# Kernel optimization log

Measured on AMD Instinct MI355X. Metric: run time of the kernel, lower is better.

The kernel has to match this reference:

```python
import jax, jax.numpy as jnp
import numpy as np

N_NODES = 50000
N_EDGES = 800000
IN_DIM = 512
HIDDEN = 512
NUM_HASH = 4
HASH_DIM = 128
NUM_GRAPHS = 64
NUM_CLASSES = 10


def _hash_mats(rng, num_hash, in_dim, hash_dim):
    # Each row of each hash matrix has a single +-1 entry at a random column.
    cols = rng.integers(0, hash_dim, size=(num_hash, in_dim))
    signs = (rng.integers(0, 2, size=(num_hash, in_dim)) * 2 - 1).astype(np.float32)
    W = np.zeros((num_hash, in_dim, hash_dim), dtype=np.float32)
    W[np.arange(num_hash)[:, None], np.arange(in_dim)[None, :], cols] = signs
    return jnp.asarray(W)


def setup_inputs() -> dict:
    key = jax.random.key(0)
    ks = jax.random.split(key, 10)
    rng = np.random.default_rng(0)
    x = jax.random.normal(ks[0], (N_NODES, IN_DIM), dtype=jnp.float32)
    edge_index = jax.random.randint(ks[1], (2, N_EDGES), 0, N_NODES, dtype=jnp.int64)
    batch = jnp.sort(jax.random.randint(ks[2], (N_NODES,), 0, NUM_GRAPHS, dtype=jnp.int64))
    s1 = 1.0 / np.sqrt(NUM_HASH * HASH_DIM)
    s2 = 1.0 / np.sqrt(IN_DIM)
    s3 = 1.0 / np.sqrt(HIDDEN)
    return {
        "x": x,
        "edge_index": edge_index,
        "batch": batch,
        "Hm1": _hash_mats(rng, NUM_HASH, IN_DIM, HASH_DIM),
        "Wp1": jax.random.normal(ks[3], (NUM_HASH * HASH_DIM, HIDDEN), dtype=jnp.float32) * s1,
        "Ws1": jax.random.normal(ks[4], (IN_DIM, HIDDEN), dtype=jnp.float32) * s2,
        "b1": jnp.zeros((HIDDEN,), dtype=jnp.float32),
        "Hm2": _hash_mats(rng, NUM_HASH, HIDDEN, HASH_DIM),
        "Wp2": jax.random.normal(ks[5], (NUM_HASH * HASH_DIM, HIDDEN), dtype=jnp.float32) * s1,
        "Ws2": jax.random.normal(ks[6], (HIDDEN, HIDDEN), dtype=jnp.float32) * s3,
        "b2": jnp.zeros((HIDDEN,), dtype=jnp.float32),
        "Wc": jax.random.normal(ks[7], (HIDDEN, NUM_CLASSES), dtype=jnp.float32) * s3,
        "bc": jnp.zeros((NUM_CLASSES,), dtype=jnp.float32),
    }


def _demo_layer(h, src, dst, deg, Hm, Wp, Ws, b):
    n = h.shape[0]
    # Degree-bucketed gather + mean == segment-mean over edges by source node.
    nsum = jax.ops.segment_sum(h[dst], src, num_segments=n)  # [N, D]
    agg = jnp.where(deg[:, None] > 0, nsum / jnp.maximum(deg, 1.0)[:, None], h)
    # Multi-hash matmul + concat: [N, K*HASH_DIM]
    hashed = jnp.einsum("nd,kdh->nkh", agg, Hm).reshape(n, -1)
    out = hashed @ Wp + h @ Ws + b
    return jax.nn.elu(out)  # dropout is identity in eval mode


def reference(x, edge_index, batch, Hm1, Wp1, Ws1, b1, Hm2, Wp2, Ws2, b2, Wc, bc):
    n = x.shape[0]
    src, dst = edge_index[0], edge_index[1]
    deg = jax.ops.segment_sum(jnp.ones(src.shape, x.dtype), src, num_segments=n)
    h = _demo_layer(x, src, dst, deg, Hm1, Wp1, Ws1, b1)
    h = _demo_layer(h, src, dst, deg, Hm2, Wp2, Ws2, b2)
    # global mean pool per graph
    cnt = jax.ops.segment_sum(jnp.ones((n,), h.dtype), batch, num_segments=NUM_GRAPHS)
    g = jax.ops.segment_sum(h, batch, num_segments=NUM_GRAPHS) / jnp.maximum(cnt, 1.0)[:, None]
    return g @ Wc + bc
```

## Files before the change

### kernel.cpp

```cpp
#include <hip/hip_runtime.h>
#include <hip/hip_bf16.h>
#include <math.h>

#define N_NODES_C 50000
#define N_EDGES_C 800000
#define DIM 512
#define NUM_GRAPHS_C 64
#define NUM_CLASSES_C 10

#define NROWT ((N_NODES_C + 127) / 128)
#define GEMM_BLOCKS (((NROWT * 4 + 31) / 32) * 32)

#define SCAN_BLK 1024
#define SCAN_NBLK ((N_NODES_C + SCAN_BLK - 1) / SCAN_BLK)

typedef short bf16x8 __attribute__((ext_vector_type(8)));
typedef float f32x4 __attribute__((ext_vector_type(4)));
typedef float f32x2 __attribute__((ext_vector_type(2)));
typedef unsigned u32x2 __attribute__((ext_vector_type(2)));

__device__ __forceinline__ float bf2f(short s) {
    return __uint_as_float(((unsigned)(unsigned short)s) << 16);
}
__device__ __forceinline__ short f2bf(float f) {
    unsigned u = __float_as_uint(f);
    u += 0x7FFF + ((u >> 16) & 1);
    return (short)(u >> 16);
}
__device__ __forceinline__ float eluf(float v) {
    return v > 0.0f ? v : expm1f(v);
}
__device__ __forceinline__ unsigned f32x4_to_fp8(float a, float b, float c, float d) {
    int w = 0;
    w = __builtin_amdgcn_cvt_pk_fp8_f32(a, b, w, false);
    w = __builtin_amdgcn_cvt_pk_fp8_f32(c, d, w, true);
    return (unsigned)w;
}
__device__ __forceinline__ unsigned char f32_to_fp8(float v) {
    return (unsigned char)(__builtin_amdgcn_cvt_pk_fp8_f32(v, v, 0, false) & 0xff);
}
__device__ __forceinline__ void acc_fp8x8(float* acc, u32x2 w) {
    f32x2 a = __builtin_amdgcn_cvt_pk_f32_fp8((int)w[0], false);
    f32x2 b = __builtin_amdgcn_cvt_pk_f32_fp8((int)w[0], true);
    f32x2 c = __builtin_amdgcn_cvt_pk_f32_fp8((int)w[1], false);
    f32x2 d = __builtin_amdgcn_cvt_pk_f32_fp8((int)w[1], true);
    acc[0] += a[0]; acc[1] += a[1]; acc[2] += b[0]; acc[3] += b[1];
    acc[4] += c[0]; acc[5] += c[1]; acc[6] += d[0]; acc[7] += d[1];
}

__device__ __forceinline__ void gl16(const void* g, void* l) {
    __builtin_amdgcn_global_load_lds(
        (const __attribute__((address_space(1))) unsigned*)g,
        (__attribute__((address_space(3))) unsigned*)l, 16, 0, 0);
}


__global__ void k_hist(const int* __restrict__ src, int* __restrict__ cnt) {
    int e = blockIdx.x * blockDim.x + threadIdx.x;
    if (e < N_EDGES_C) atomicAdd(&cnt[src[e]], 1);
}

__global__ __launch_bounds__(1024)
void k_bsum(const int* __restrict__ cnt, int* __restrict__ bsum) {
    __shared__ int sh[1024];
    int i = blockIdx.x * 1024 + threadIdx.x;
    sh[threadIdx.x] = (i < N_NODES_C) ? cnt[i] : 0;
    __syncthreads();
    for (int ofs = 512; ofs > 0; ofs >>= 1) {
        if ((int)threadIdx.x < ofs) sh[threadIdx.x] += sh[threadIdx.x + ofs];
        __syncthreads();
    }
    if (threadIdx.x == 0) bsum[blockIdx.x] = sh[0];
}

__global__ __launch_bounds__(64)
void k_bscan(const int* __restrict__ bsum, int* __restrict__ bofs,
             int* __restrict__ start) {
    int l = threadIdx.x;
    int own = (l < SCAN_NBLK) ? bsum[l] : 0;
    int v = own;
    for (int ofs = 1; ofs < 64; ofs <<= 1) {
        int t = __shfl_up(v, ofs, 64);
        if (l >= ofs) v += t;
    }
    if (l < SCAN_NBLK) bofs[l] = v - own;
    if (l == 63) start[N_NODES_C] = v;
}

__global__ __launch_bounds__(1024)
void k_scan_apply(const int* __restrict__ cnt, const int* __restrict__ bofs,
                  int* __restrict__ start, int* __restrict__ cursor) {
    __shared__ int sh[1024];
    int i = blockIdx.x * 1024 + threadIdx.x;
    int v = (i < N_NODES_C) ? cnt[i] : 0;
    sh[threadIdx.x] = v;
    __syncthreads();
    for (int ofs = 1; ofs < 1024; ofs <<= 1) {
        int t = (threadIdx.x >= (unsigned)ofs) ? sh[threadIdx.x - ofs] : 0;
        __syncthreads();
        sh[threadIdx.x] += t;
        __syncthreads();
    }
    if (i < N_NODES_C) {
        int ex = bofs[blockIdx.x] + sh[threadIdx.x] - v;
        start[i] = ex;
        cursor[i] = ex;
    }
}

__global__ void k_fill(const int* __restrict__ src, const int* __restrict__ dst,
                       int* __restrict__ cursor, int* __restrict__ ebuf) {
    int e = blockIdx.x * blockDim.x + threadIdx.x;
    if (e < N_EDGES_C) {
        int pos = atomicAdd(&cursor[src[e]], 1);
        ebuf[pos] = dst[e];
    }
}

__global__ __launch_bounds__(1024)
void k_cnt(const int* __restrict__ batch, int* __restrict__ cnt) {
    __shared__ int h[NUM_GRAPHS_C];
    if (threadIdx.x < NUM_GRAPHS_C) h[threadIdx.x] = 0;
    __syncthreads();
    int n = blockIdx.x * blockDim.x + threadIdx.x;
    if (n < N_NODES_C) {
        int g = batch[n];
        if ((unsigned)g < NUM_GRAPHS_C) atomicAdd(&h[g], 1);
    }
    __syncthreads();
    if (threadIdx.x < NUM_GRAPHS_C && h[threadIdx.x] > 0)
        atomicAdd(&cnt[threadIdx.x], h[threadIdx.x]);
}

__global__ void k_weff(const float* __restrict__ Hm, const float* __restrict__ Wp,
                       float* __restrict__ Weff) {
    __shared__ int   scol[4];
    __shared__ float ssign[4];
    int d = blockIdx.x;
    int h = threadIdx.x;
    for (int k = 0; k < 4; ++k) {
        float v = Hm[((size_t)k * DIM + d) * 128 + h];
        if (v != 0.0f) { scol[k] = h; ssign[k] = v; }
    }
    __syncthreads();
    for (int j = threadIdx.x; j < DIM; j += 128) {
        float acc = 0.0f;
#pragma unroll
        for (int k = 0; k < 4; ++k)
            acc += ssign[k] * Wp[(size_t)(k * 128 + scol[k]) * DIM + j];
        Weff[(size_t)d * DIM + j] = acc;
    }
}

__global__ void k_prepw(const float* __restrict__ Weff, const float* __restrict__ Ws,
                        short* __restrict__ Wt) {
    int n = blockIdx.x;
    for (int k = threadIdx.x; k < 2 * DIM; k += 256) {
        float v = (k < DIM) ? Weff[(size_t)k * DIM + n] : Ws[(size_t)(k - DIM) * DIM + n];
        Wt[(size_t)n * (2 * DIM) + k] = f2bf(v);
    }
}

__global__ void k_cast(const float* __restrict__ x, short* __restrict__ xb,
                       unsigned char* __restrict__ xq) {
    int idx = blockIdx.x * blockDim.x + threadIdx.x;
    if (idx >= N_NODES_C * DIM / 8) return;
    const float* p = x + (size_t)idx * 8;
    float v[8];
    bf16x8 o;
#pragma unroll
    for (int j = 0; j < 8; ++j) { v[j] = p[j]; o[j] = f2bf(v[j]); }
    u32x2 q;
    q[0] = f32x4_to_fp8(v[0], v[1], v[2], v[3]);
    q[1] = f32x4_to_fp8(v[4], v[5], v[6], v[7]);
    *(bf16x8*)(xb + (size_t)idx * 8) = o;
    *(u32x2*)(xq + (size_t)idx * 8) = q;
}

__global__ __launch_bounds__(256)
void k_gather_8(const unsigned char* __restrict__ Hq, const int* __restrict__ start,
                const int* __restrict__ ebuf, const short* __restrict__ fb,
                short* __restrict__ outb) {
    int n = blockIdx.x * 4 + (threadIdx.x >> 6);
    int l = threadIdx.x & 63;
    if (n >= N_NODES_C) return;
    int s = start[n], e = start[n + 1];
    float acc[8] = {0, 0, 0, 0, 0, 0, 0, 0};
    int i = s;
    if (i + 4 <= e) {
        int d0 = ebuf[i], d1 = ebuf[i + 1], d2 = ebuf[i + 2], d3 = ebuf[i + 3];
        for (; i + 8 <= e; i += 4) {
            int n0 = ebuf[i + 4], n1 = ebuf[i + 5], n2 = ebuf[i + 6], n3 = ebuf[i + 7];
            u32x2 w0 = *(const u32x2*)(Hq + (size_t)d0 * DIM + l * 8);
            u32x2 w1 = *(const u32x2*)(Hq + (size_t)d1 * DIM + l * 8);
            u32x2 w2 = *(const u32x2*)(Hq + (size_t)d2 * DIM + l * 8);
            u32x2 w3 = *(const u32x2*)(Hq + (size_t)d3 * DIM + l * 8);
            acc_fp8x8(acc, w0); acc_fp8x8(acc, w1);
            acc_fp8x8(acc, w2); acc_fp8x8(acc, w3);
            d0 = n0; d1 = n1; d2 = n2; d3 = n3;
        }
        {
            u32x2 w0 = *(const u32x2*)(Hq + (size_t)d0 * DIM + l * 8);
            u32x2 w1 = *(const u32x2*)(Hq + (size_t)d1 * DIM + l * 8);
            u32x2 w2 = *(const u32x2*)(Hq + (size_t)d2 * DIM + l * 8);
            u32x2 w3 = *(const u32x2*)(Hq + (size_t)d3 * DIM + l * 8);
            acc_fp8x8(acc, w0); acc_fp8x8(acc, w1);
            acc_fp8x8(acc, w2); acc_fp8x8(acc, w3);
            i += 4;
        }
    }
    for (; i < e; ++i) {
        int d0 = ebuf[i];
        u32x2 w0 = *(const u32x2*)(Hq + (size_t)d0 * DIM + l * 8);
        acc_fp8x8(acc, w0);
    }
    bf16x8 o;
    if (e > s) {
        float inv = 1.0f / (float)(e - s);
#pragma unroll
        for (int j = 0; j < 8; ++j) o[j] = f2bf(acc[j] * inv);
    } else {
        o = *(const bf16x8*)(fb + (size_t)n * DIM + l * 8);
    }
    *(bf16x8*)(outb + (size_t)n * DIM + l * 8) = o;
}


__device__ __forceinline__ void gemm_core(const short* __restrict__ A1,
                                          const short* __restrict__ A2,
                                          const short* __restrict__ Wt,
                                          short* As, short* Bs,
                                          int row0, int col0,
                                          int wave, int lane, f32x4 (*acc)[4]) {
    const int wm = wave >> 1, wn = wave & 1;
    const int q = lane >> 4, t16 = lane & 15;
    const int rloc = wave * 32 + (lane >> 3);
    const int csrc = (lane & 7) ^ (lane >> 3);
    size_t aoff[4], boff[4];
#pragma unroll
    for (int j = 0; j < 4; ++j) {
        int grow = row0 + rloc + j * 8;
        if (grow >= N_NODES_C) grow = N_NODES_C - 1;
        aoff[j] = (size_t)grow * DIM + csrc * 8;
        boff[j] = (size_t)(col0 + rloc + j * 8) * (2 * DIM) + csrc * 8;
    }
    short* AsW = As + wave * 2048;
    short* BsW = Bs + wave * 2048;
#pragma unroll
    for (int p = 0; p < 2; ++p) {
        const short* A = p ? A2 : A1;
        const short* W = Wt + p * DIM;
        for (int kt = 0; kt < DIM; kt += 64) {
            __syncthreads();
#pragma unroll
            for (int j = 0; j < 4; ++j) {
                gl16(A + aoff[j] + kt, AsW + j * 512);
                gl16(W + boff[j] + kt, BsW + j * 512);
            }
            __syncthreads();
#pragma unroll
            for (int kh = 0; kh < 2; ++kh) {
                bf16x8 af[4], bfv[4];
#pragma unroll
                for (int mi = 0; mi < 4; ++mi) {
                    int r = wm * 64 + mi * 16 + t16;
                    int cp = (kh * 4 + q) ^ (t16 & 7);
                    af[mi] = *(const bf16x8*)(As + r * 64 + cp * 8);
                }
#pragma unroll
                for (int ni = 0; ni < 4; ++ni) {
                    int r = wn * 64 + ni * 16 + t16;
                    int cp = (kh * 4 + q) ^ (t16 & 7);
                    bfv[ni] = *(const bf16x8*)(Bs + r * 64 + cp * 8);
                }
#pragma unroll
                for (int mi = 0; mi < 4; ++mi)
#pragma unroll
                    for (int ni = 0; ni < 4; ++ni)
                        acc[mi][ni] = __builtin_amdgcn_mfma_f32_16x16x32_bf16(
                            af[mi], bfv[ni], acc[mi][ni], 0, 0, 0);
            }
        }
    }
}

__global__ __launch_bounds__(256, 4)
void k_gemm_elu_mfma(const short* __restrict__ A1, const short* __restrict__ A2,
                     const short* __restrict__ Wt, const float* __restrict__ bias,
                     short* __restrict__ C, unsigned char* __restrict__ C8) {
    __shared__ __align__(16) short As[128 * 64];
    __shared__ __align__(16) short Bs[128 * 64];
    const int L = blockIdx.x;
    const int ct = (L & 31) >> 3;
    const int rt = ((L >> 5) << 3) + (L & 7);
    if (rt >= NROWT) return;
    const int row0 = rt * 128, col0 = ct * 128;
    const int tid = threadIdx.x;
    const int lane = tid & 63, wave = tid >> 6;
    const int wm = wave >> 1, wn = wave & 1;
    const int q = lane >> 4, t16 = lane & 15;
    f32x4 acc[4][4] = {};
    gemm_core(A1, A2, Wt, As, Bs, row0, col0, wave, lane, acc);
#pragma unroll
    for (int mi = 0; mi < 4; ++mi) {
        int rbase = row0 + wm * 64 + mi * 16 + q * 4;
#pragma unroll
        for (int ni = 0; ni < 4; ++ni) {
            int col = col0 + wn * 64 + ni * 16 + t16;
            float bj = bias[col];
#pragma unroll
            for (int r = 0; r < 4; ++r) {
                int row = rbase + r;
                if (row < N_NODES_C) {
                    float v = eluf(acc[mi][ni][r] + bj);
                    C[(size_t)row * DIM + col] = f2bf(v);
                    C8[(size_t)row * DIM + col] = f32_to_fp8(v);
                }
            }
        }
    }
}

__global__ __launch_bounds__(256, 4)
void k_gemm_pool_mfma(const short* __restrict__ A1, const short* __restrict__ A2,
                      const short* __restrict__ Wt, const float* __restrict__ bias,
                      const int* __restrict__ batch, float* __restrict__ gsum) {
    __shared__ __align__(16) short As[128 * 64];
    __shared__ __align__(16) short Bs[128 * 64];
    __shared__ int sbatch[128];
    const int L = blockIdx.x;
    const int ct = (L & 31) >> 3;
    const int rt = ((L >> 5) << 3) + (L & 7);
    if (rt >= NROWT) return;
    const int row0 = rt * 128, col0 = ct * 128;
    const int tid = threadIdx.x;
    const int lane = tid & 63, wave = tid >> 6;
    const int wm = wave >> 1, wn = wave & 1;
    const int q = lane >> 4, t16 = lane & 15;
    if (tid < 128) {
        int rw = row0 + tid;
        sbatch[tid] = (rw < N_NODES_C) ? batch[rw] : -1;
    }
    f32x4 acc[4][4] = {};
    gemm_core(A1, A2, Wt, As, Bs, row0, col0, wave, lane, acc);
    const int tb = wm * 64 + q * 4;
    const int g0 = sbatch[tb];
    const int g3 = sbatch[tb + 51];
    if (g0 == g3) {
        if (g0 >= 0) {
#pragma unroll
            for (int ni = 0; ni < 4; ++ni) {
                int col = col0 + wn * 64 + ni * 16 + t16;
                float bj = bias[col];
                float s = 0.0f;
#pragma unroll
                for (int mi = 0; mi < 4; ++mi)
#pragma unroll
                    for (int r = 0; r < 4; ++r)
                        s += eluf(acc[mi][ni][r] + bj);
                atomicAdd(&gsum[(size_t)g0 * DIM + col], s);
            }
        }
    } else {
#pragma unroll
        for (int mi = 0; mi < 4; ++mi) {
            int rb = tb + mi * 16;
#pragma unroll
            for (int ni = 0; ni < 4; ++ni) {
                int col = col0 + wn * 64 + ni * 16 + t16;
                float bj = bias[col];
                int curg = -1;
                float run = 0.0f;
#pragma unroll
                for (int r = 0; r < 4; ++r) {
                    int g = sbatch[rb + r];
                    if (g < 0) break;
                    float v = eluf(acc[mi][ni][r] + bj);
                    if (g != curg) {
                        if (curg >= 0) atomicAdd(&gsum[(size_t)curg * DIM + col], run);
                        curg = g;
                        run = 0.0f;
                    }
                    run += v;
                }
                if (curg >= 0) atomicAdd(&gsum[(size_t)curg * DIM + col], run);
            }
        }
    }
}

__global__ void k_final(const float* __restrict__ gsum, const int* __restrict__ cnt,
                        const float* __restrict__ Wc, const float* __restrict__ bc,
                        float* __restrict__ out) {
    int g = blockIdx.x;
    int j = threadIdx.x;
    if (j >= NUM_CLASSES_C) return;
    int c_ = cnt[g];
    float inv = 1.0f / (float)(c_ > 1 ? c_ : 1);
    float s = 0.0f;
    for (int c = 0; c < DIM; ++c)
        s += gsum[(size_t)g * DIM + c] * Wc[(size_t)c * NUM_CLASSES_C + j];
    out[g * NUM_CLASSES_C + j] = s * inv + bc[j];
}


extern "C" void kernel_launch(void* const* d_in, const int* in_sizes, int n_in,
                              void* d_out, int out_size, void* d_ws, size_t ws_size,
                              hipStream_t stream) {
    const float* x   = (const float*)d_in[0];
    const int*   ei  = (const int*)d_in[1];
    const int*   src = ei;
    const int*   dst = ei + N_EDGES_C;
    const int* batch = (const int*)d_in[2];
    const float* Hm1 = (const float*)d_in[3];
    const float* Wp1 = (const float*)d_in[4];
    const float* Ws1 = (const float*)d_in[5];
    const float* b1  = (const float*)d_in[6];
    const float* Hm2 = (const float*)d_in[7];
    const float* Wp2 = (const float*)d_in[8];
    const float* Ws2 = (const float*)d_in[9];
    const float* b2  = (const float*)d_in[10];
    const float* Wc  = (const float*)d_in[11];
    const float* bc  = (const float*)d_in[12];
    float* out = (float*)d_out;

    char* ws = (char*)d_ws;
    size_t off = 0;
    auto alloc = [&](size_t bytes) {
        void* p = ws + off;
        off += (bytes + 255) & ~(size_t)255;
        return p;
    };
    const size_t nodeB16 = (size_t)N_NODES_C * DIM * 2;
    const size_t nodeB8  = (size_t)N_NODES_C * DIM;
    short* xb    = (short*)alloc(nodeB16);
    short* aggB  = (short*)alloc(nodeB16);
    short* hB    = (short*)alloc(nodeB16);
    unsigned char* xq = (unsigned char*)alloc(nodeB8);
    unsigned char* hq = (unsigned char*)alloc(nodeB8);
    float* Weff1 = (float*)alloc((size_t)DIM * DIM * 4);
    float* Weff2 = (float*)alloc((size_t)DIM * DIM * 4);
    short* Wt1   = (short*)alloc((size_t)DIM * 2 * DIM * 2);
    short* Wt2   = (short*)alloc((size_t)DIM * 2 * DIM * 2);
    int*   cnt_i = (int*)alloc((size_t)N_NODES_C * 4);
    int*   start = (int*)alloc((size_t)(N_NODES_C + 1) * 4);
    int*   cursor= (int*)alloc((size_t)N_NODES_C * 4);
    int*   ebuf  = (int*)alloc((size_t)N_EDGES_C * 4);
    int*   cnt   = (int*)alloc((size_t)NUM_GRAPHS_C * 4);
    float* gsum  = (float*)alloc((size_t)NUM_GRAPHS_C * DIM * 4);
    int*   bsum  = (int*)alloc((size_t)SCAN_NBLK * 4);
    int*   bofs  = (int*)alloc((size_t)SCAN_NBLK * 4);

    hipMemsetAsync(cnt_i, 0, (size_t)N_NODES_C * 4, stream);
    hipMemsetAsync(cnt, 0, (size_t)NUM_GRAPHS_C * 4, stream);
    hipMemsetAsync(gsum, 0, (size_t)NUM_GRAPHS_C * DIM * 4, stream);

    k_hist<<<(N_EDGES_C + 255) / 256, 256, 0, stream>>>(src, cnt_i);
    k_bsum<<<SCAN_NBLK, 1024, 0, stream>>>(cnt_i, bsum);
    k_bscan<<<1, 64, 0, stream>>>(bsum, bofs, start);
    k_scan_apply<<<SCAN_NBLK, 1024, 0, stream>>>(cnt_i, bofs, start, cursor);
    k_fill<<<(N_EDGES_C + 255) / 256, 256, 0, stream>>>(src, dst, cursor, ebuf);
    k_cnt<<<(N_NODES_C + 1023) / 1024, 1024, 0, stream>>>(batch, cnt);
    k_weff<<<DIM, 128, 0, stream>>>(Hm1, Wp1, Weff1);
    k_weff<<<DIM, 128, 0, stream>>>(Hm2, Wp2, Weff2);
    k_prepw<<<DIM, 256, 0, stream>>>(Weff1, Ws1, Wt1);
    k_prepw<<<DIM, 256, 0, stream>>>(Weff2, Ws2, Wt2);
    k_cast<<<(N_NODES_C * DIM / 8 + 255) / 256, 256, 0, stream>>>(x, xb, xq);

    k_gather_8<<<(N_NODES_C + 3) / 4, 256, 0, stream>>>(xq, start, ebuf, xb, aggB);
    k_gemm_elu_mfma<<<GEMM_BLOCKS, 256, 0, stream>>>(aggB, xb, Wt1, b1, hB, hq);

    k_gather_8<<<(N_NODES_C + 3) / 4, 256, 0, stream>>>(hq, start, ebuf, hB, aggB);
    k_gemm_pool_mfma<<<GEMM_BLOCKS, 256, 0, stream>>>(aggB, hB, Wt2, b2, batch, gsum);

    k_final<<<NUM_GRAPHS_C, 64, 0, stream>>>(gsum, cnt, Wc, bc, out);
}
```

Before: 615.2 us.

## Double-buffer LDS tiles in MFMA GEMM core to overlap loads with compute

The GEMM core now keeps two LDS buffers for the A and B tiles and issues the global-to-LDS loads for the next K stage while running MFMAs on the current one. This replaces the two barriers per stage with one. The two K passes (aggregate and self features) are merged into a single 16-stage loop. In exchange, LDS use per block doubles and launch bounds drop from 4 to 2 blocks per CU, which lowers occupancy.

```diff
diff --git a/kernel.cpp b/kernel.cpp
--- a/kernel.cpp
+++ b/kernel.cpp
@@ -246,50 +246,61 @@
     }
     short* AsW = As + wave * 2048;
     short* BsW = Bs + wave * 2048;
-#pragma unroll
-    for (int p = 0; p < 2; ++p) {
-        const short* A = p ? A2 : A1;
-        const short* W = Wt + p * DIM;
-        for (int kt = 0; kt < DIM; kt += 64) {
-            __syncthreads();
-#pragma unroll
-            for (int j = 0; j < 4; ++j) {
-                gl16(A + aoff[j] + kt, AsW + j * 512);
-                gl16(W + boff[j] + kt, BsW + j * 512);
+
+#define STAGE(s, buf)                                                         \
+    {                                                                         \
+        const short* Ap_ = ((s) >= 8) ? A2 : A1;                              \
+        const short* Wp_ = Wt + (((s) >= 8) ? DIM : 0);                       \
+        const int kt_ = ((s) & 7) * 64;                                       \
+        _Pragma("unroll")                                                     \
+        for (int j = 0; j < 4; ++j) {                                         \
+            gl16(Ap_ + aoff[j] + kt_, AsW + (buf) * 8192 + j * 512);          \
+            gl16(Wp_ + boff[j] + kt_, BsW + (buf) * 8192 + j * 512);          \
+        }                                                                     \
+    }
+
+    STAGE(0, 0);
+    __syncthreads();
+    int cur = 0;
+#pragma unroll 2
+    for (int s = 0; s < 16; ++s) {
+        if (s < 15) STAGE(s + 1, cur ^ 1);
+        const short* Ab = As + cur * 8192;
+        const short* Bb = Bs + cur * 8192;
+#pragma unroll
+        for (int kh = 0; kh < 2; ++kh) {
+            bf16x8 af[4], bfv[4];
+#pragma unroll
+            for (int mi = 0; mi < 4; ++mi) {
+                int r = wm * 64 + mi * 16 + t16;
+                int cp = (kh * 4 + q) ^ (t16 & 7);
+                af[mi] = *(const bf16x8*)(Ab + r * 64 + cp * 8);
             }
-            __syncthreads();
-#pragma unroll
-            for (int kh = 0; kh < 2; ++kh) {
-                bf16x8 af[4], bfv[4];
-#pragma unroll
-                for (int mi = 0; mi < 4; ++mi) {
-                    int r = wm * 64 + mi * 16 + t16;
-                    int cp = (kh * 4 + q) ^ (t16 & 7);
-                    af[mi] = *(const bf16x8*)(As + r * 64 + cp * 8);
-                }
-#pragma unroll
-                for (int ni = 0; ni < 4; ++ni) {
-                    int r = wn * 64 + ni * 16 + t16;
-                    int cp = (kh * 4 + q) ^ (t16 & 7);
-                    bfv[ni] = *(const bf16x8*)(Bs + r * 64 + cp * 8);
-                }
-#pragma unroll
-                for (int mi = 0; mi < 4; ++mi)
-#pragma unroll
-                    for (int ni = 0; ni < 4; ++ni)
-                        acc[mi][ni] = __builtin_amdgcn_mfma_f32_16x16x32_bf16(
-                            af[mi], bfv[ni], acc[mi][ni], 0, 0, 0);
+#pragma unroll
+            for (int ni = 0; ni < 4; ++ni) {
+                int r = wn * 64 + ni * 16 + t16;
+                int cp = (kh * 4 + q) ^ (t16 & 7);
+                bfv[ni] = *(const bf16x8*)(Bb + r * 64 + cp * 8);
             }
-        }
-    }
-}
-
-__global__ __launch_bounds__(256, 4)
+#pragma unroll
+            for (int mi = 0; mi < 4; ++mi)
+#pragma unroll
+                for (int ni = 0; ni < 4; ++ni)
+                    acc[mi][ni] = __builtin_amdgcn_mfma_f32_16x16x32_bf16(
+                        af[mi], bfv[ni], acc[mi][ni], 0, 0, 0);
+        }
+        __syncthreads();
+        cur ^= 1;
+    }
+#undef STAGE
+}
+
+__global__ __launch_bounds__(256, 2)
 void k_gemm_elu_mfma(const short* __restrict__ A1, const short* __restrict__ A2,
                      const short* __restrict__ Wt, const float* __restrict__ bias,
                      short* __restrict__ C, unsigned char* __restrict__ C8) {
-    __shared__ __align__(16) short As[128 * 64];
-    __shared__ __align__(16) short Bs[128 * 64];
+    __shared__ __align__(16) short As[2 * 128 * 64];
+    __shared__ __align__(16) short Bs[2 * 128 * 64];
     const int L = blockIdx.x;
     const int ct = (L & 31) >> 3;
     const int rt = ((L >> 5) << 3) + (L & 7);
@@ -321,12 +332,12 @@
     }
 }
 
-__global__ __launch_bounds__(256, 4)
+__global__ __launch_bounds__(256, 2)
 void k_gemm_pool_mfma(const short* __restrict__ A1, const short* __restrict__ A2,
                       const short* __restrict__ Wt, const float* __restrict__ bias,
                       const int* __restrict__ batch, float* __restrict__ gsum) {
-    __shared__ __align__(16) short As[128 * 64];
-    __shared__ __align__(16) short Bs[128 * 64];
+    __shared__ __align__(16) short As[2 * 128 * 64];
+    __shared__ __align__(16) short Bs[2 * 128 * 64];
     __shared__ int sbatch[128];
     const int L = blockIdx.x;
     const int ct = (L & 31) >> 3;
```

Result: slower. 700.6 us (+13.9%).
